# Kernel tuning notes

Measured on AMD Instinct MI355X. Metric: run time of the kernel, lower is better.

Reference implementation:

```python
import jax, jax.numpy as jnp
import numpy as np

N, E, D, C = 50000, 800000, 96, 40
L2_EPS = 1e-12  # tf.nn.l2_normalize epsilon


def setup_inputs() -> dict:
    key = jax.random.key(0)
    ks = jax.random.split(key, 8)
    row = jnp.sort(jax.random.randint(ks[0], (E,), 0, N, dtype=jnp.int32))
    col = jax.random.randint(ks[1], (E,), 0, N, dtype=jnp.int32)
    vals = jax.random.uniform(ks[2], (E,), dtype=jnp.float32)
    x = jax.random.normal(ks[3], (N, D), dtype=jnp.float32)
    w1 = jax.random.normal(ks[4], (D, D), dtype=jnp.float32) * 0.1
    w2 = jax.random.normal(ks[5], (D, D), dtype=jnp.float32) * 0.1
    wc = jax.random.normal(ks[6], (D, C), dtype=jnp.float32) * 0.1
    bc = jnp.zeros((C,), dtype=jnp.float32)
    return {"row": row, "col": col, "vals": vals, "x": x,
            "w1": w1, "w2": w2, "wc": wc, "bc": bc}


def _spmm(row, col, vals, h):
    # sparse A (coo: row, col, vals) @ dense h, via gather + segment_sum
    msg = vals[:, None] * h[col]            # [E, D]
    return jax.ops.segment_sum(msg, row, num_segments=N)


def reference(row, col, vals, x, w1, w2, wc, bc):
    h = x
    for w in (w1, w2):                       # GCNConv: act(A @ (h @ W)), no bias
        h = jax.nn.relu(_spmm(row, col, vals, h @ w))
    # tf.nn.l2_normalize(h, axis=1)
    sq = jnp.sum(h * h, axis=1, keepdims=True)
    out = h * jax.lax.rsqrt(jnp.maximum(sq, L2_EPS))
    probs = jax.nn.softmax(out @ wc + bc, axis=-1)
    return out, probs
```

## Files before the change

kernel.cpp:

```cpp
#include <hip/hip_runtime.h>
#include <hip/hip_bf16.h>

#define GN 50000
#define GE 800000
#define GD 96
#define GC 40
#define L2EPS 1e-12f

typedef __attribute__((ext_vector_type(8))) short short8v;
typedef __attribute__((ext_vector_type(4))) float f32x4;

__device__ __forceinline__ unsigned f2bf(float x) {
    union { float f; unsigned u; } v; v.f = x;
    return (v.u + 0x7fffu + ((v.u >> 16) & 1u)) >> 16;
}
__device__ __forceinline__ float bflo(unsigned u) { return __uint_as_float(u << 16); }
__device__ __forceinline__ float bfhi(unsigned u) { return __uint_as_float(u & 0xffff0000u); }

__device__ __forceinline__ int lbound(const int* __restrict__ row, int key) {
    int lo = 0, hi = GE;
    while (lo < hi) {
        int mid = (lo + hi) >> 1;
        if (row[mid] < key) lo = mid + 1; else hi = mid;
    }
    return lo;
}

__global__ void prep_k(const int* __restrict__ row, const float* __restrict__ w1,
                       const float* __restrict__ w2, int* __restrict__ rp,
                       unsigned* __restrict__ Wb1, unsigned* __restrict__ Wb2) {
    int i = blockIdx.x * blockDim.x + threadIdx.x;
    if (i <= GN) rp[i] = lbound(row, i);
    if (i < 2 * 4608) {
        const float* W = (i < 4608) ? w1 : w2;
        unsigned* Wb   = (i < 4608) ? Wb1 : Wb2;
        int j = (i < 4608) ? i : i - 4608;
        int r = j & 3;
        int lane = (j >> 2) & 63;
        int frag = j >> 8;
        int nt = frag / 3, kt = frag - nt * 3;
        int c = nt * 16 + (lane & 15);
        int k = kt * 32 + (lane >> 4) * 8 + r * 2;
        Wb[j] = f2bf(W[k * GD + c]) | (f2bf(W[(k + 1) * GD + c]) << 16);
    }
}

__global__ __launch_bounds__(64) void gemm_mfma_k(const float* __restrict__ A,
                                                  const uint4* __restrict__ Wb,
                                                  unsigned short* __restrict__ O) {
    const int tile = blockIdx.x;
    const int l  = threadIdx.x;
    const int m  = l & 15;
    const int kg = l >> 4;

    const float* arow = A + (size_t)(tile * 16 + m) * GD + kg * 8;
    short8v ah[3], al[3];
#pragma unroll
    for (int kt = 0; kt < 3; ++kt) {
        const float4* ap = reinterpret_cast<const float4*>(arow + kt * 32);
        float4 x0 = ap[0], x1 = ap[1];
        uint4 H, L;
        H.x = f2bf(x0.x) | (f2bf(x0.y) << 16);
        H.y = f2bf(x0.z) | (f2bf(x0.w) << 16);
        H.z = f2bf(x1.x) | (f2bf(x1.y) << 16);
        H.w = f2bf(x1.z) | (f2bf(x1.w) << 16);
        L.x = f2bf(x0.x - bflo(H.x)) | (f2bf(x0.y - bfhi(H.x)) << 16);
        L.y = f2bf(x0.z - bflo(H.y)) | (f2bf(x0.w - bfhi(H.y)) << 16);
        L.z = f2bf(x1.x - bflo(H.z)) | (f2bf(x1.y - bfhi(H.z)) << 16);
        L.w = f2bf(x1.z - bflo(H.w)) | (f2bf(x1.w - bfhi(H.w)) << 16);
        union { uint4 u; short8v s; } ch, cl;
        ch.u = H; cl.u = L;
        ah[kt] = ch.s; al[kt] = cl.s;
    }

#pragma unroll
    for (int nt = 0; nt < 6; ++nt) {
        f32x4 acc = {0.f, 0.f, 0.f, 0.f};
#pragma unroll
        for (int kt = 0; kt < 3; ++kt) {
            union { uint4 u; short8v s; } b;
            b.u = Wb[(nt * 3 + kt) * 64 + l];
            acc = __builtin_amdgcn_mfma_f32_16x16x32_bf16(ah[kt], b.s, acc, 0, 0, 0);
            acc = __builtin_amdgcn_mfma_f32_16x16x32_bf16(al[kt], b.s, acc, 0, 0, 0);
        }
        int ccol = nt * 16 + m;
#pragma unroll
        for (int reg = 0; reg < 4; ++reg) {
            int rrow = tile * 16 + kg * 4 + reg;
            O[(size_t)rrow * GD + ccol] = (unsigned short)f2bf(acc[reg]);
        }
    }
}

#define FMA8(U, V)                                                    \
    a0 += (V) * bflo((U).x); a1 += (V) * bfhi((U).x);                 \
    a2 += (V) * bflo((U).y); a3 += (V) * bfhi((U).y);                 \
    a4 += (V) * bflo((U).z); a5 += (V) * bfhi((U).z);                 \
    a6 += (V) * bflo((U).w); a7 += (V) * bfhi((U).w);

__global__ void spmm_relu_k(const int* __restrict__ rp, const int* __restrict__ col,
                            const float* __restrict__ vals,
                            const unsigned* __restrict__ Tb, float* __restrict__ H) {
    int idx = blockIdx.x * blockDim.x + threadIdx.x;
    int n = idx / 12;
    if (n >= GN) return;
    int t = idx - n * 12;
    int e0 = rp[n], e1 = rp[n + 1];
    float a0=0,a1=0,a2=0,a3=0,a4=0,a5=0,a6=0,a7=0;
    int e = e0;
    for (; e + 4 <= e1; e += 4) {
        int c0 = col[e], c1 = col[e+1], c2 = col[e+2], c3 = col[e+3];
        float v0 = vals[e], v1 = vals[e+1], v2 = vals[e+2], v3 = vals[e+3];
        uint4 u0 = *reinterpret_cast<const uint4*>(Tb + (size_t)c0 * 48 + t * 4);
        uint4 u1 = *reinterpret_cast<const uint4*>(Tb + (size_t)c1 * 48 + t * 4);
        uint4 u2 = *reinterpret_cast<const uint4*>(Tb + (size_t)c2 * 48 + t * 4);
        uint4 u3 = *reinterpret_cast<const uint4*>(Tb + (size_t)c3 * 48 + t * 4);
        FMA8(u0, v0) FMA8(u1, v1) FMA8(u2, v2) FMA8(u3, v3)
    }
    for (; e < e1; ++e) {
        float v = vals[e];
        uint4 u = *reinterpret_cast<const uint4*>(Tb + (size_t)col[e] * 48 + t * 4);
        FMA8(u, v)
    }
    float4* hr = reinterpret_cast<float4*>(H + (size_t)n * GD + t * 8);
    hr[0] = make_float4(fmaxf(a0,0.f), fmaxf(a1,0.f), fmaxf(a2,0.f), fmaxf(a3,0.f));
    hr[1] = make_float4(fmaxf(a4,0.f), fmaxf(a5,0.f), fmaxf(a6,0.f), fmaxf(a7,0.f));
}

#define FMA12(U, W_, V)                                               \
    a0 += (V) * bflo((U).x); a1 += (V) * bfhi((U).x);                 \
    a2 += (V) * bflo((U).y); a3 += (V) * bfhi((U).y);                 \
    a4 += (V) * bflo((U).z); a5 += (V) * bfhi((U).z);                 \
    a6 += (V) * bflo((U).w); a7 += (V) * bfhi((U).w);                 \
    a8 += (V) * bflo((W_).x); a9 += (V) * bfhi((W_).x);               \
    a10 += (V) * bflo((W_).y); a11 += (V) * bfhi((W_).y);

__global__ void spmm_relu_norm_k(const int* __restrict__ rp, const int* __restrict__ col,
                                 const float* __restrict__ vals,
                                 const unsigned* __restrict__ Tb, float* __restrict__ H) {
    int idx = blockIdx.x * blockDim.x + threadIdx.x;
    int n = idx >> 3;
    if (n >= GN) return;
    int t = idx & 7;
    int e0 = rp[n], e1 = rp[n + 1];
    float a0=0,a1=0,a2=0,a3=0,a4=0,a5=0,a6=0,a7=0,a8=0,a9=0,a10=0,a11=0;
    int e = e0;
    for (; e + 4 <= e1; e += 4) {
        int c0 = col[e], c1 = col[e+1], c2 = col[e+2], c3 = col[e+3];
        float v0 = vals[e], v1 = vals[e+1], v2 = vals[e+2], v3 = vals[e+3];
        const unsigned* r0p = Tb + (size_t)c0 * 48;
        const unsigned* r1p = Tb + (size_t)c1 * 48;
        const unsigned* r2p = Tb + (size_t)c2 * 48;
        const unsigned* r3p = Tb + (size_t)c3 * 48;
        uint4 u0 = *reinterpret_cast<const uint4*>(r0p + t * 4);
        uint2 w0 = *reinterpret_cast<const uint2*>(r0p + 32 + t * 2);
        uint4 u1 = *reinterpret_cast<const uint4*>(r1p + t * 4);
        uint2 w1 = *reinterpret_cast<const uint2*>(r1p + 32 + t * 2);
        uint4 u2 = *reinterpret_cast<const uint4*>(r2p + t * 4);
        uint2 w2 = *reinterpret_cast<const uint2*>(r2p + 32 + t * 2);
        uint4 u3 = *reinterpret_cast<const uint4*>(r3p + t * 4);
        uint2 w3 = *reinterpret_cast<const uint2*>(r3p + 32 + t * 2);
        FMA12(u0, w0, v0) FMA12(u1, w1, v1) FMA12(u2, w2, v2) FMA12(u3, w3, v3)
    }
    for (; e < e1; ++e) {
        float v = vals[e];
        const unsigned* r = Tb + (size_t)col[e] * 48;
        uint4 u = *reinterpret_cast<const uint4*>(r + t * 4);
        uint2 w = *reinterpret_cast<const uint2*>(r + 32 + t * 2);
        FMA12(u, w, v)
    }
    a0=fmaxf(a0,0.f); a1=fmaxf(a1,0.f); a2=fmaxf(a2,0.f); a3=fmaxf(a3,0.f);
    a4=fmaxf(a4,0.f); a5=fmaxf(a5,0.f); a6=fmaxf(a6,0.f); a7=fmaxf(a7,0.f);
    a8=fmaxf(a8,0.f); a9=fmaxf(a9,0.f); a10=fmaxf(a10,0.f); a11=fmaxf(a11,0.f);
    float ss = a0*a0+a1*a1+a2*a2+a3*a3+a4*a4+a5*a5+a6*a6+a7*a7+a8*a8+a9*a9+a10*a10+a11*a11;
    ss += __shfl_xor(ss, 1);
    ss += __shfl_xor(ss, 2);
    ss += __shfl_xor(ss, 4);
    float s = rsqrtf(fmaxf(ss, L2EPS));
    a0*=s; a1*=s; a2*=s; a3*=s; a4*=s; a5*=s;
    a6*=s; a7*=s; a8*=s; a9*=s; a10*=s; a11*=s;
    float4* hr = reinterpret_cast<float4*>(H + (size_t)n * GD + t * 8);
    hr[0] = make_float4(a0, a1, a2, a3);
    hr[1] = make_float4(a4, a5, a6, a7);
    *reinterpret_cast<float4*>(H + (size_t)n * GD + 64 + t * 4) =
        make_float4(a8, a9, a10, a11);
}

__global__ __launch_bounds__(320) void cls_sm_k(const float* __restrict__ A,
                                                const float* __restrict__ WC,
                                                const float* __restrict__ BC,
                                                float* __restrict__ PROBS) {
    __shared__ float4 w4[GD * 10];
    __shared__ float lg[128][GC];
    const float4* W4 = reinterpret_cast<const float4*>(WC);
    for (int i = threadIdx.x; i < GD * 10; i += 320) w4[i] = W4[i];
    __syncthreads();

    const int tid = threadIdx.x;
    const int lq = tid / 10;
    const int q  = tid - lq * 10;
    const int r0 = (blockIdx.x * 32 + lq) * 4;
    if (r0 < GN) {
        const float* a = A + (size_t)r0 * GD;
        float4 acc0 = {0,0,0,0}, acc1 = {0,0,0,0}, acc2 = {0,0,0,0}, acc3 = {0,0,0,0};
        for (int k0 = 0; k0 < GD; k0 += 4) {
            float4 a0 = *reinterpret_cast<const float4*>(a + k0);
            float4 a1 = *reinterpret_cast<const float4*>(a + GD + k0);
            float4 a2 = *reinterpret_cast<const float4*>(a + 2 * GD + k0);
            float4 a3 = *reinterpret_cast<const float4*>(a + 3 * GD + k0);
#pragma unroll
            for (int kk = 0; kk < 4; ++kk) {
                float4 w = w4[(k0 + kk) * 10 + q];
                float s0 = ((const float*)&a0)[kk];
                float s1 = ((const float*)&a1)[kk];
                float s2 = ((const float*)&a2)[kk];
                float s3 = ((const float*)&a3)[kk];
                acc0.x += s0 * w.x; acc0.y += s0 * w.y; acc0.z += s0 * w.z; acc0.w += s0 * w.w;
                acc1.x += s1 * w.x; acc1.y += s1 * w.y; acc1.z += s1 * w.z; acc1.w += s1 * w.w;
                acc2.x += s2 * w.x; acc2.y += s2 * w.y; acc2.z += s2 * w.z; acc2.w += s2 * w.w;
                acc3.x += s3 * w.x; acc3.y += s3 * w.y; acc3.z += s3 * w.z; acc3.w += s3 * w.w;
            }
        }
        float4 b = *reinterpret_cast<const float4*>(BC + q * 4);
        acc0.x += b.x; acc0.y += b.y; acc0.z += b.z; acc0.w += b.w;
        acc1.x += b.x; acc1.y += b.y; acc1.z += b.z; acc1.w += b.w;
        acc2.x += b.x; acc2.y += b.y; acc2.z += b.z; acc2.w += b.w;
        acc3.x += b.x; acc3.y += b.y; acc3.z += b.z; acc3.w += b.w;
        *reinterpret_cast<float4*>(&lg[lq * 4 + 0][q * 4]) = acc0;
        *reinterpret_cast<float4*>(&lg[lq * 4 + 1][q * 4]) = acc1;
        *reinterpret_cast<float4*>(&lg[lq * 4 + 2][q * 4]) = acc2;
        *reinterpret_cast<float4*>(&lg[lq * 4 + 3][q * 4]) = acc3;
    }
    __syncthreads();

    if (tid < 128) {
        int r = blockIdx.x * 128 + tid;
        if (r < GN) {
            const float* row = lg[tid];
            float m = row[0];
#pragma unroll
            for (int c = 1; c < GC; ++c) m = fmaxf(m, row[c]);
            float ex[GC];
            float sum = 0.f;
#pragma unroll
            for (int c = 0; c < GC; ++c) { ex[c] = __expf(row[c] - m); sum += ex[c]; }
            float inv = 1.f / sum;
            float4* pr = reinterpret_cast<float4*>(PROBS + (size_t)r * GC);
#pragma unroll
            for (int i = 0; i < 10; ++i)
                pr[i] = make_float4(ex[i*4] * inv, ex[i*4+1] * inv,
                                    ex[i*4+2] * inv, ex[i*4+3] * inv);
        }
    }
}

extern "C" void kernel_launch(void* const* d_in, const int* in_sizes, int n_in,
                              void* d_out, int out_size, void* d_ws, size_t ws_size,
                              hipStream_t stream) {
    const int*   row  = (const int*)d_in[0];
    const int*   col  = (const int*)d_in[1];
    const float* vals = (const float*)d_in[2];
    const float* x    = (const float*)d_in[3];
    const float* w1   = (const float*)d_in[4];
    const float* w2   = (const float*)d_in[5];
    const float* wc   = (const float*)d_in[6];
    const float* bc   = (const float*)d_in[7];

    float* out   = (float*)d_out;
    float* probs = out + (size_t)GN * GD;

    char*  ws  = (char*)d_ws;
    int*   rp  = (int*)ws;
    size_t off = (((size_t)(GN + 1) * 4) + 511) & ~(size_t)511;
    unsigned* buf = (unsigned*)(ws + off);
    off += (size_t)GN * GD * 4;
    off = (off + 511) & ~(size_t)511;
    unsigned* Wb1 = (unsigned*)(ws + off);
    unsigned* Wb2 = Wb1 + 4608;

    prep_k<<<(GN + 1 + 255) / 256, 256, 0, stream>>>(row, w1, w2, rp, Wb1, Wb2);
    gemm_mfma_k<<<GN / 16, 64, 0, stream>>>(x, (const uint4*)Wb1, (unsigned short*)buf);
    spmm_relu_k<<<(GN * 12 + 255) / 256, 256, 0, stream>>>(rp, col, vals, buf, out);
    gemm_mfma_k<<<GN / 16, 64, 0, stream>>>(out, (const uint4*)Wb2, (unsigned short*)buf);
    spmm_relu_norm_k<<<(GN * 8 + 255) / 256, 256, 0, stream>>>(rp, col, vals, buf, out);
    cls_sm_k<<<(GN + 127) / 128, 320, 0, stream>>>(out, wc, bc, probs);
}
```

Baseline: 101.7 us.

## Split bf16 feature table into column halves and move L2 norm into classifier

The GEMM now writes its bf16 output as two separate column-half tables (48 columns each). Each SpMM runs as two passes, one per half, so each gather working set is half the size and more likely to stay in L2/MALL cache. The L2 normalization moves out of the second SpMM into the classifier kernel, which computes row norms, scales the logits, and writes the normalized rows back in place. The cost is twice as many SpMM launches that re-read col/vals/rowptr, and the classifier now does an extra pass over the rows plus the write-back.

```diff
diff --git a/kernel.cpp b/kernel.cpp
--- a/kernel.cpp
+++ b/kernel.cpp
@@ -83,110 +83,50 @@
             acc = __builtin_amdgcn_mfma_f32_16x16x32_bf16(ah[kt], b.s, acc, 0, 0, 0);
             acc = __builtin_amdgcn_mfma_f32_16x16x32_bf16(al[kt], b.s, acc, 0, 0, 0);
         }
-        int ccol = nt * 16 + m;
+        unsigned short* dst = O + ((nt < 3) ? 0 : (size_t)GN * 48);
+        int ccol = (nt % 3) * 16 + m;
 #pragma unroll
         for (int reg = 0; reg < 4; ++reg) {
             int rrow = tile * 16 + kg * 4 + reg;
-            O[(size_t)rrow * GD + ccol] = (unsigned short)f2bf(acc[reg]);
-        }
-    }
-}
-
-#define FMA8(U, V)                                                    \
+            dst[(size_t)rrow * 48 + ccol] = (unsigned short)f2bf(acc[reg]);
+        }
+    }
+}
+
+#define FMA4(U, V)                                                    \
     a0 += (V) * bflo((U).x); a1 += (V) * bfhi((U).x);                 \
-    a2 += (V) * bflo((U).y); a3 += (V) * bfhi((U).y);                 \
-    a4 += (V) * bflo((U).z); a5 += (V) * bfhi((U).z);                 \
-    a6 += (V) * bflo((U).w); a7 += (V) * bfhi((U).w);
-
-__global__ void spmm_relu_k(const int* __restrict__ rp, const int* __restrict__ col,
+    a2 += (V) * bflo((U).y); a3 += (V) * bfhi((U).y);
+
+__global__ void spmm_half_k(const int* __restrict__ rp, const int* __restrict__ col,
                             const float* __restrict__ vals,
-                            const unsigned* __restrict__ Tb, float* __restrict__ H) {
+                            const unsigned* __restrict__ Tb, float* __restrict__ H,
+                            int colOff) {
     int idx = blockIdx.x * blockDim.x + threadIdx.x;
     int n = idx / 12;
     if (n >= GN) return;
     int t = idx - n * 12;
     int e0 = rp[n], e1 = rp[n + 1];
-    float a0=0,a1=0,a2=0,a3=0,a4=0,a5=0,a6=0,a7=0;
+    float a0=0,a1=0,a2=0,a3=0;
     int e = e0;
     for (; e + 4 <= e1; e += 4) {
         int c0 = col[e], c1 = col[e+1], c2 = col[e+2], c3 = col[e+3];
         float v0 = vals[e], v1 = vals[e+1], v2 = vals[e+2], v3 = vals[e+3];
-        uint4 u0 = *reinterpret_cast<const uint4*>(Tb + (size_t)c0 * 48 + t * 4);
-        uint4 u1 = *reinterpret_cast<const uint4*>(Tb + (size_t)c1 * 48 + t * 4);
-        uint4 u2 = *reinterpret_cast<const uint4*>(Tb + (size_t)c2 * 48 + t * 4);
-        uint4 u3 = *reinterpret_cast<const uint4*>(Tb + (size_t)c3 * 48 + t * 4);
-        FMA8(u0, v0) FMA8(u1, v1) FMA8(u2, v2) FMA8(u3, v3)
+        uint2 u0 = *reinterpret_cast<const uint2*>(Tb + (size_t)c0 * 24 + t * 2);
+        uint2 u1 = *reinterpret_cast<const uint2*>(Tb + (size_t)c1 * 24 + t * 2);
+        uint2 u2 = *reinterpret_cast<const uint2*>(Tb + (size_t)c2 * 24 + t * 2);
+        uint2 u3 = *reinterpret_cast<const uint2*>(Tb + (size_t)c3 * 24 + t * 2);
+        FMA4(u0, v0) FMA4(u1, v1) FMA4(u2, v2) FMA4(u3, v3)
     }
     for (; e < e1; ++e) {
         float v = vals[e];
-        uint4 u = *reinterpret_cast<const uint4*>(Tb + (size_t)col[e] * 48 + t * 4);
-        FMA8(u, v)
-    }
-    float4* hr = reinterpret_cast<float4*>(H + (size_t)n * GD + t * 8);
-    hr[0] = make_float4(fmaxf(a0,0.f), fmaxf(a1,0.f), fmaxf(a2,0.f), fmaxf(a3,0.f));
-    hr[1] = make_float4(fmaxf(a4,0.f), fmaxf(a5,0.f), fmaxf(a6,0.f), fmaxf(a7,0.f));
-}
-
-#define FMA12(U, W_, V)                                               \
-    a0 += (V) * bflo((U).x); a1 += (V) * bfhi((U).x);                 \
-    a2 += (V) * bflo((U).y); a3 += (V) * bfhi((U).y);                 \
-    a4 += (V) * bflo((U).z); a5 += (V) * bfhi((U).z);                 \
-    a6 += (V) * bflo((U).w); a7 += (V) * bfhi((U).w);                 \
-    a8 += (V) * bflo((W_).x); a9 += (V) * bfhi((W_).x);               \
-    a10 += (V) * bflo((W_).y); a11 += (V) * bfhi((W_).y);
-
-__global__ void spmm_relu_norm_k(const int* __restrict__ rp, const int* __restrict__ col,
-                                 const float* __restrict__ vals,
-                                 const unsigned* __restrict__ Tb, float* __restrict__ H) {
-    int idx = blockIdx.x * blockDim.x + threadIdx.x;
-    int n = idx >> 3;
-    if (n >= GN) return;
-    int t = idx & 7;
-    int e0 = rp[n], e1 = rp[n + 1];
-    float a0=0,a1=0,a2=0,a3=0,a4=0,a5=0,a6=0,a7=0,a8=0,a9=0,a10=0,a11=0;
-    int e = e0;
-    for (; e + 4 <= e1; e += 4) {
-        int c0 = col[e], c1 = col[e+1], c2 = col[e+2], c3 = col[e+3];
-        float v0 = vals[e], v1 = vals[e+1], v2 = vals[e+2], v3 = vals[e+3];
-        const unsigned* r0p = Tb + (size_t)c0 * 48;
-        const unsigned* r1p = Tb + (size_t)c1 * 48;
-        const unsigned* r2p = Tb + (size_t)c2 * 48;
-        const unsigned* r3p = Tb + (size_t)c3 * 48;
-        uint4 u0 = *reinterpret_cast<const uint4*>(r0p + t * 4);
-        uint2 w0 = *reinterpret_cast<const uint2*>(r0p + 32 + t * 2);
-        uint4 u1 = *reinterpret_cast<const uint4*>(r1p + t * 4);
-        uint2 w1 = *reinterpret_cast<const uint2*>(r1p + 32 + t * 2);
-        uint4 u2 = *reinterpret_cast<const uint4*>(r2p + t * 4);
-        uint2 w2 = *reinterpret_cast<const uint2*>(r2p + 32 + t * 2);
-        uint4 u3 = *reinterpret_cast<const uint4*>(r3p + t * 4);
-        uint2 w3 = *reinterpret_cast<const uint2*>(r3p + 32 + t * 2);
-        FMA12(u0, w0, v0) FMA12(u1, w1, v1) FMA12(u2, w2, v2) FMA12(u3, w3, v3)
-    }
-    for (; e < e1; ++e) {
-        float v = vals[e];
-        const unsigned* r = Tb + (size_t)col[e] * 48;
-        uint4 u = *reinterpret_cast<const uint4*>(r + t * 4);
-        uint2 w = *reinterpret_cast<const uint2*>(r + 32 + t * 2);
-        FMA12(u, w, v)
-    }
-    a0=fmaxf(a0,0.f); a1=fmaxf(a1,0.f); a2=fmaxf(a2,0.f); a3=fmaxf(a3,0.f);
-    a4=fmaxf(a4,0.f); a5=fmaxf(a5,0.f); a6=fmaxf(a6,0.f); a7=fmaxf(a7,0.f);
-    a8=fmaxf(a8,0.f); a9=fmaxf(a9,0.f); a10=fmaxf(a10,0.f); a11=fmaxf(a11,0.f);
-    float ss = a0*a0+a1*a1+a2*a2+a3*a3+a4*a4+a5*a5+a6*a6+a7*a7+a8*a8+a9*a9+a10*a10+a11*a11;
-    ss += __shfl_xor(ss, 1);
-    ss += __shfl_xor(ss, 2);
-    ss += __shfl_xor(ss, 4);
-    float s = rsqrtf(fmaxf(ss, L2EPS));
-    a0*=s; a1*=s; a2*=s; a3*=s; a4*=s; a5*=s;
-    a6*=s; a7*=s; a8*=s; a9*=s; a10*=s; a11*=s;
-    float4* hr = reinterpret_cast<float4*>(H + (size_t)n * GD + t * 8);
-    hr[0] = make_float4(a0, a1, a2, a3);
-    hr[1] = make_float4(a4, a5, a6, a7);
-    *reinterpret_cast<float4*>(H + (size_t)n * GD + 64 + t * 4) =
-        make_float4(a8, a9, a10, a11);
-}
-
-__global__ __launch_bounds__(320) void cls_sm_k(const float* __restrict__ A,
+        uint2 u = *reinterpret_cast<const uint2*>(Tb + (size_t)col[e] * 24 + t * 2);
+        FMA4(u, v)
+    }
+    *reinterpret_cast<float4*>(H + (size_t)n * GD + colOff + t * 4) =
+        make_float4(fmaxf(a0,0.f), fmaxf(a1,0.f), fmaxf(a2,0.f), fmaxf(a3,0.f));
+}
+
+__global__ __launch_bounds__(320) void cls_sm_k(float* __restrict__ A,
                                                 const float* __restrict__ WC,
                                                 const float* __restrict__ BC,
                                                 float* __restrict__ PROBS) {
@@ -201,31 +141,48 @@
     const int q  = tid - lq * 10;
     const int r0 = (blockIdx.x * 32 + lq) * 4;
     if (r0 < GN) {
-        const float* a = A + (size_t)r0 * GD;
+        float4* a4 = reinterpret_cast<float4*>(A + (size_t)r0 * GD);
+        float ss0=0.f, ss1=0.f, ss2=0.f, ss3=0.f;
+#pragma unroll 6
+        for (int i = 0; i < 24; ++i) {
+            float4 v0 = a4[i], v1 = a4[24+i], v2 = a4[48+i], v3 = a4[72+i];
+            ss0 += v0.x*v0.x + v0.y*v0.y + v0.z*v0.z + v0.w*v0.w;
+            ss1 += v1.x*v1.x + v1.y*v1.y + v1.z*v1.z + v1.w*v1.w;
+            ss2 += v2.x*v2.x + v2.y*v2.y + v2.z*v2.z + v2.w*v2.w;
+            ss3 += v3.x*v3.x + v3.y*v3.y + v3.z*v3.z + v3.w*v3.w;
+        }
+        float s0 = rsqrtf(fmaxf(ss0, L2EPS));
+        float s1 = rsqrtf(fmaxf(ss1, L2EPS));
+        float s2 = rsqrtf(fmaxf(ss2, L2EPS));
+        float s3 = rsqrtf(fmaxf(ss3, L2EPS));
+
         float4 acc0 = {0,0,0,0}, acc1 = {0,0,0,0}, acc2 = {0,0,0,0}, acc3 = {0,0,0,0};
-        for (int k0 = 0; k0 < GD; k0 += 4) {
-            float4 a0 = *reinterpret_cast<const float4*>(a + k0);
-            float4 a1 = *reinterpret_cast<const float4*>(a + GD + k0);
-            float4 a2 = *reinterpret_cast<const float4*>(a + 2 * GD + k0);
-            float4 a3 = *reinterpret_cast<const float4*>(a + 3 * GD + k0);
+        for (int i = 0; i < 24; ++i) {
+            float4 a0 = a4[i], a1 = a4[24+i], a2 = a4[48+i], a3 = a4[72+i];
+            if (i % 10 == q) {
+                a4[i]    = make_float4(a0.x*s0, a0.y*s0, a0.z*s0, a0.w*s0);
+                a4[24+i] = make_float4(a1.x*s1, a1.y*s1, a1.z*s1, a1.w*s1);
+                a4[48+i] = make_float4(a2.x*s2, a2.y*s2, a2.z*s2, a2.w*s2);
+                a4[72+i] = make_float4(a3.x*s3, a3.y*s3, a3.z*s3, a3.w*s3);
+            }
 #pragma unroll
             for (int kk = 0; kk < 4; ++kk) {
-                float4 w = w4[(k0 + kk) * 10 + q];
-                float s0 = ((const float*)&a0)[kk];
-                float s1 = ((const float*)&a1)[kk];
-                float s2 = ((const float*)&a2)[kk];
-                float s3 = ((const float*)&a3)[kk];
-                acc0.x += s0 * w.x; acc0.y += s0 * w.y; acc0.z += s0 * w.z; acc0.w += s0 * w.w;
-                acc1.x += s1 * w.x; acc1.y += s1 * w.y; acc1.z += s1 * w.z; acc1.w += s1 * w.w;
-                acc2.x += s2 * w.x; acc2.y += s2 * w.y; acc2.z += s2 * w.z; acc2.w += s2 * w.w;
-                acc3.x += s3 * w.x; acc3.y += s3 * w.y; acc3.z += s3 * w.z; acc3.w += s3 * w.w;
+                float4 w = w4[(i * 4 + kk) * 10 + q];
+                float t0 = ((const float*)&a0)[kk];
+                float t1 = ((const float*)&a1)[kk];
+                float t2 = ((const float*)&a2)[kk];
+                float t3 = ((const float*)&a3)[kk];
+                acc0.x += t0 * w.x; acc0.y += t0 * w.y; acc0.z += t0 * w.z; acc0.w += t0 * w.w;
+                acc1.x += t1 * w.x; acc1.y += t1 * w.y; acc1.z += t1 * w.z; acc1.w += t1 * w.w;
+                acc2.x += t2 * w.x; acc2.y += t2 * w.y; acc2.z += t2 * w.z; acc2.w += t2 * w.w;
+                acc3.x += t3 * w.x; acc3.y += t3 * w.y; acc3.z += t3 * w.z; acc3.w += t3 * w.w;
             }
         }
         float4 b = *reinterpret_cast<const float4*>(BC + q * 4);
-        acc0.x += b.x; acc0.y += b.y; acc0.z += b.z; acc0.w += b.w;
-        acc1.x += b.x; acc1.y += b.y; acc1.z += b.z; acc1.w += b.w;
-        acc2.x += b.x; acc2.y += b.y; acc2.z += b.z; acc2.w += b.w;
-        acc3.x += b.x; acc3.y += b.y; acc3.z += b.z; acc3.w += b.w;
+        acc0.x = acc0.x*s0 + b.x; acc0.y = acc0.y*s0 + b.y; acc0.z = acc0.z*s0 + b.z; acc0.w = acc0.w*s0 + b.w;
+        acc1.x = acc1.x*s1 + b.x; acc1.y = acc1.y*s1 + b.y; acc1.z = acc1.z*s1 + b.z; acc1.w = acc1.w*s1 + b.w;
+        acc2.x = acc2.x*s2 + b.x; acc2.y = acc2.y*s2 + b.y; acc2.z = acc2.z*s2 + b.z; acc2.w = acc2.w*s2 + b.w;
+        acc3.x = acc3.x*s3 + b.x; acc3.y = acc3.y*s3 + b.y; acc3.z = acc3.z*s3 + b.z; acc3.w = acc3.w*s3 + b.w;
         *reinterpret_cast<float4*>(&lg[lq * 4 + 0][q * 4]) = acc0;
         *reinterpret_cast<float4*>(&lg[lq * 4 + 1][q * 4]) = acc1;
         *reinterpret_cast<float4*>(&lg[lq * 4 + 2][q * 4]) = acc2;
@@ -272,16 +229,22 @@
     char*  ws  = (char*)d_ws;
     int*   rp  = (int*)ws;
     size_t off = (((size_t)(GN + 1) * 4) + 511) & ~(size_t)511;
-    unsigned* buf = (unsigned*)(ws + off);
-    off += (size_t)GN * GD * 4;
+    unsigned short* tb = (unsigned short*)(ws + off);
+    off += (size_t)GN * GD * 2;
     off = (off + 511) & ~(size_t)511;
     unsigned* Wb1 = (unsigned*)(ws + off);
     unsigned* Wb2 = Wb1 + 4608;
 
+    const unsigned* tlo = (const unsigned*)tb;
+    const unsigned* thi = (const unsigned*)(tb + (size_t)GN * 48);
+    const int spmm_blocks = (GN * 12 + 255) / 256;
+
     prep_k<<<(GN + 1 + 255) / 256, 256, 0, stream>>>(row, w1, w2, rp, Wb1, Wb2);
-    gemm_mfma_k<<<GN / 16, 64, 0, stream>>>(x, (const uint4*)Wb1, (unsigned short*)buf);
-    spmm_relu_k<<<(GN * 12 + 255) / 256, 256, 0, stream>>>(rp, col, vals, buf, out);
-    gemm_mfma_k<<<GN / 16, 64, 0, stream>>>(out, (const uint4*)Wb2, (unsigned short*)buf);
-    spmm_relu_norm_k<<<(GN * 8 + 255) / 256, 256, 0, stream>>>(rp, col, vals, buf, out);
+    gemm_mfma_k<<<GN / 16, 64, 0, stream>>>(x, (const uint4*)Wb1, tb);
+    spmm_half_k<<<spmm_blocks, 256, 0, stream>>>(rp, col, vals, tlo, out, 0);
+    spmm_half_k<<<spmm_blocks, 256, 0, stream>>>(rp, col, vals, thi, out, 48);
+    gemm_mfma_k<<<GN / 16, 64, 0, stream>>>(out, (const uint4*)Wb2, tb);
+    spmm_half_k<<<spmm_blocks, 256, 0, stream>>>(rp, col, vals, tlo, out, 0);
+    spmm_half_k<<<spmm_blocks, 256, 0, stream>>>(rp, col, vals, thi, out, 48);
     cls_sm_k<<<(GN + 127) / 128, 320, 0, stream>>>(out, wc, bc, probs);
 }
```

Result: slower. 137.4 us (+35.1%).
